# Kernel tuning notes

Measured on AMD Instinct MI355X. Metric: run time of the kernel, lower is better.

The kernel has to match this reference:

```python
import jax, jax.numpy as jnp
import numpy as np

H = 32
W = 32
DIM = 64  # per-head dim; c = DIM // 2


def _rel_idx(n):
    coords = jnp.arange(n)
    return coords[None, :] - coords[:, None] + (n - 1)  # [n, n] in [0, 2n-2]


def setup_inputs() -> dict:
    key = jax.random.key(0)
    k1, k2, k3, k4 = jax.random.split(key, 4)
    B, G = 8, 8
    q = jax.random.normal(k1, (B, H * W, G, DIM), dtype=jnp.float32)
    attn = jax.random.normal(k2, (B, H * W, G, H * W), dtype=jnp.float32)
    c = DIM // 2
    rel_emb_h = jax.random.normal(k3, (2 * H - 1, c), dtype=jnp.float32) * 0.02
    rel_emb_w = jax.random.normal(k4, (2 * W - 1, c), dtype=jnp.float32) * 0.02
    return {"q": q, "attn": attn, "rel_emb_h": rel_emb_h, "rel_emb_w": rel_emb_w}


def reference(q, attn, rel_emb_h, rel_emb_w):
    B, QL, G, D = q.shape
    c = D // 2
    # gather relative-position embeddings: [h, h, c] and [w, w, c]
    abs_pos_h = rel_emb_h[_rel_idx(H)]
    abs_pos_w = rel_emb_w[_rel_idx(W)]
    # split q into (h, w) grid and two channel halves: [B, h, w, G, 2, c]
    qg = q.reshape(B, H, W, G, 2, c)
    logits_h = jnp.einsum('bhwgc,hkc->bhwgk', qg[..., 0, :], abs_pos_h)  # [B,h,w,G,h]
    logits_w = jnp.einsum('bhwgc,wkc->bhwgk', qg[..., 1, :], abs_pos_w)  # [B,h,w,G,w]
    # broadcast-add into attn viewed as [B, q, G, kh, kw]
    a = attn.reshape(B, QL, G, H, W)
    a = a + logits_h.reshape(B, QL, G, H, 1) + logits_w.reshape(B, QL, G, 1, W)
    return a.reshape(B, QL, G, H * W)
```

## Files before the change

kernel.cpp:

```cpp
#include <hip/hip_runtime.h>


#define QL 1024

typedef float floatx4 __attribute__((ext_vector_type(4)));

__global__ __launch_bounds__(256) void relpos_fused2_kernel(
    const float* __restrict__ q,
    const float* __restrict__ attn,
    const float* __restrict__ reh,
    const float* __restrict__ rew,
    float* __restrict__ out,
    int ntasks)
{
    const int lane = threadIdx.x & 63;
    const int wid  = blockIdx.x * 4 + (threadIdx.x >> 6);
    const int nwaves = gridDim.x * 4;

    for (int t = wid; t < ntasks; t += nwaves) {
        const int hw = t & (QL - 1);
        const int h  = hw >> 5;
        const int w  = hw & 31;
        const size_t r0 = (size_t)t << 3;

        const int k = lane & 31;
        const float4* e4 = (lane < 32)
            ? (const float4*)(reh + (size_t)(k - h + 31) * 32)
            : (const float4*)(rew + (size_t)(k - w + 31) * 32);
        const float* qbase = q + r0 * 64 + (lane & 32);

        float acc[8];
        #pragma unroll
        for (int g = 0; g < 8; ++g) acc[g] = 0.f;
        #pragma unroll
        for (int c4 = 0; c4 < 8; ++c4) {
            const float4 ev = e4[c4];
            #pragma unroll
            for (int g = 0; g < 8; ++g) {
                const float4 qv = *(const float4*)(qbase + g * 64 + c4 * 4);
                acc[g] += qv.x * ev.x + qv.y * ev.y + qv.z * ev.z + qv.w * ev.w;
            }
        }

        const int kw0 = (lane << 2) & 31;
        const int kh0 = lane >> 3;
        float lh[8][4], lw[8][4];
        #pragma unroll
        for (int g = 0; g < 8; ++g) {
            const float a = acc[g];
            lh[g][0] = __shfl(a, kh0,      64);
            lh[g][1] = __shfl(a, kh0 + 8,  64);
            lh[g][2] = __shfl(a, kh0 + 16, 64);
            lh[g][3] = __shfl(a, kh0 + 24, 64);
            lw[g][0] = __shfl(a, 32 + kw0,     64);
            lw[g][1] = __shfl(a, 32 + kw0 + 1, 64);
            lw[g][2] = __shfl(a, 32 + kw0 + 2, 64);
            lw[g][3] = __shfl(a, 32 + kw0 + 3, 64);
        }

        const float4* abase = (const float4*)(attn + r0 * QL);
        floatx4*      obase = (floatx4*)(out  + r0 * QL);

        float4 buf[2][4];
        #pragma unroll
        for (int j = 0; j < 4; ++j)
            buf[0][j] = abase[lane + 64 * j];

        #pragma unroll
        for (int g = 0; g < 8; ++g) {
            if (g < 7) {
                const float4* anext = abase + (size_t)(g + 1) * 256;
                #pragma unroll
                for (int j = 0; j < 4; ++j)
                    buf[(g + 1) & 1][j] = anext[lane + 64 * j];
            }
            floatx4* orow = obase + (size_t)g * 256;
            #pragma unroll
            for (int j = 0; j < 4; ++j) {
                const float4 a = buf[g & 1][j];
                const float tl = lh[g][j];
                floatx4 o;
                o.x = a.x + tl + lw[g][0];
                o.y = a.y + tl + lw[g][1];
                o.z = a.z + tl + lw[g][2];
                o.w = a.w + tl + lw[g][3];
                __builtin_nontemporal_store(o, &orow[lane + 64 * j]);
            }
        }
    }
}

extern "C" void kernel_launch(void* const* d_in, const int* in_sizes, int n_in,
                              void* d_out, int out_size, void* d_ws, size_t ws_size,
                              hipStream_t stream) {
    const float* q    = (const float*)d_in[0];
    const float* attn = (const float*)d_in[1];
    const float* reh  = (const float*)d_in[2];
    const float* rew  = (const float*)d_in[3];
    float* out = (float*)d_out;

    const int nrows  = in_sizes[1] / QL;
    const int ntasks = nrows >> 3;
    relpos_fused2_kernel<<<2048, 256, 0, stream>>>(q, attn, reh, rew, out, ntasks);
}
```

Before: 111.4 us.

## Split fused kernel into logits precompute and attn streaming kernels

```diff
diff --git a/kernel.cpp b/kernel.cpp
--- a/kernel.cpp
+++ b/kernel.cpp
@@ -4,6 +4,85 @@
 #define QL 1024
 
 typedef float floatx4 __attribute__((ext_vector_type(4)));
+
+__global__ __launch_bounds__(256) void logits_kernel(
+    const float* __restrict__ q,
+    const float* __restrict__ reh,
+    const float* __restrict__ rew,
+    float* __restrict__ lg,
+    int ntasks)
+{
+    const int lane = threadIdx.x & 63;
+    const int wid  = blockIdx.x * 4 + (threadIdx.x >> 6);
+    const int nwaves = gridDim.x * 4;
+
+    for (int t = wid; t < ntasks; t += nwaves) {
+        const int hw = t & (QL - 1);
+        const int h  = hw >> 5;
+        const int w  = hw & 31;
+        const size_t r0 = (size_t)t << 3;
+
+        const int k = lane & 31;
+        const float4* e4 = (lane < 32)
+            ? (const float4*)(reh + (size_t)(k - h + 31) * 32)
+            : (const float4*)(rew + (size_t)(k - w + 31) * 32);
+        const float* qbase = q + r0 * 64 + (lane & 32);
+
+        float acc[8];
+        #pragma unroll
+        for (int g = 0; g < 8; ++g) acc[g] = 0.f;
+        #pragma unroll
+        for (int c4 = 0; c4 < 8; ++c4) {
+            const float4 ev = e4[c4];
+            #pragma unroll
+            for (int g = 0; g < 8; ++g) {
+                const float4 qv = *(const float4*)(qbase + g * 64 + c4 * 4);
+                acc[g] += qv.x * ev.x + qv.y * ev.y + qv.z * ev.z + qv.w * ev.w;
+            }
+        }
+        #pragma unroll
+        for (int g = 0; g < 8; ++g)
+            lg[(r0 + g) * 64 + lane] = acc[g];
+    }
+}
+
+__global__ __launch_bounds__(256) void stream_kernel(
+    const float* __restrict__ attn,
+    const float* __restrict__ lg,
+    float* __restrict__ out,
+    int nrows)
+{
+    const int u   = threadIdx.x;
+    const int kh  = u >> 3;
+    const int kw4 = (u & 7) * 4;
+
+    const int rstep = gridDim.x * 2;
+    for (int rb = blockIdx.x * 2; rb < nrows; rb += rstep) {
+        const float4* a0 = (const float4*)(attn + (size_t)rb * QL);
+        const float4* a1 = (const float4*)(attn + (size_t)(rb + 1) * QL);
+        const float*  l0 = lg + (size_t)rb * 64;
+        const float*  l1 = lg + (size_t)(rb + 1) * 64;
+
+        const float4 av0 = a0[u];
+        const float4 av1 = a1[u];
+        const float  lh0 = l0[kh];
+        const float  lh1 = l1[kh];
+        const float4 lw0 = *(const float4*)(l0 + 32 + kw4);
+        const float4 lw1 = *(const float4*)(l1 + 32 + kw4);
+
+        floatx4 o;
+        o.x = av0.x + lh0 + lw0.x;
+        o.y = av0.y + lh0 + lw0.y;
+        o.z = av0.z + lh0 + lw0.z;
+        o.w = av0.w + lh0 + lw0.w;
+        __builtin_nontemporal_store(o, (floatx4*)(out + (size_t)rb * QL) + u);
+        o.x = av1.x + lh1 + lw1.x;
+        o.y = av1.y + lh1 + lw1.y;
+        o.z = av1.z + lh1 + lw1.z;
+        o.w = av1.w + lh1 + lw1.w;
+        __builtin_nontemporal_store(o, (floatx4*)(out + (size_t)(rb + 1) * QL) + u);
+    }
+}
 
 __global__ __launch_bounds__(256) void relpos_fused2_kernel(
     const float* __restrict__ q,
@@ -41,7 +120,6 @@
                 acc[g] += qv.x * ev.x + qv.y * ev.y + qv.z * ev.z + qv.w * ev.w;
             }
         }
-
         const int kw0 = (lane << 2) & 31;
         const int kh0 = lane >> 3;
         float lh[8][4], lw[8][4];
@@ -57,15 +135,12 @@
             lw[g][2] = __shfl(a, 32 + kw0 + 2, 64);
             lw[g][3] = __shfl(a, 32 + kw0 + 3, 64);
         }
-
         const float4* abase = (const float4*)(attn + r0 * QL);
         floatx4*      obase = (floatx4*)(out  + r0 * QL);
-
         float4 buf[2][4];
         #pragma unroll
         for (int j = 0; j < 4; ++j)
             buf[0][j] = abase[lane + 64 * j];
-
         #pragma unroll
         for (int g = 0; g < 8; ++g) {
             if (g < 7) {
@@ -101,5 +176,13 @@
 
     const int nrows  = in_sizes[1] / QL;
     const int ntasks = nrows >> 3;
-    relpos_fused2_kernel<<<2048, 256, 0, stream>>>(q, attn, reh, rew, out, ntasks);
+
+    const size_t lg_bytes = (size_t)nrows * 64 * sizeof(float);
+    if (ws_size >= lg_bytes) {
+        float* lg = (float*)d_ws;
+        logits_kernel<<<2048, 256, 0, stream>>>(q, reh, rew, lg, ntasks);
+        stream_kernel<<<2048, 256, 0, stream>>>(attn, lg, out, nrows);
+    } else {
+        relpos_fused2_kernel<<<2048, 256, 0, stream>>>(q, attn, reh, rew, out, ntasks);
+    }
 }
```

Result: slower. 119.2 us (+7.0%).
